# Kernel optimization log

Hardware: AMD Instinct MI355X
Metric: run time of the kernel (lower is better)

The kernel has to match this reference:

```python
import jax, jax.numpy as jnp
import numpy as np

PROJ_EPS = 4e-3      # geoopt-style Poincare projection margin (float32)
MIN_NORM = 1e-15
ATANH_EPS = 1e-5     # clamp arg of arctanh away from 1
WEI_EPS = 1e-3       # self.eps buffer
P_EXP = 2.0          # self.p buffer


def _project(v, k):
    # Project onto Poincare ball of curvature -k: clip norm to (1-eps)/sqrt(k).
    # k has shape (1,H,1,1), v has shape (B,H,T,D).
    maxnorm = (1.0 - PROJ_EPS) / jnp.sqrt(k)
    norm = jnp.sqrt(jnp.clip(jnp.sum(v * v, axis=-1, keepdims=True), MIN_NORM))
    return jnp.where(norm > maxnorm, v / norm * maxnorm, v)


def setup_inputs() -> dict:
    key = jax.random.key(0)
    k1, k2, k3, k4 = jax.random.split(key, 4)
    B, T, C, H = 4, 1024, 768, 12
    x = jax.random.normal(k1, (B, T, C), dtype=jnp.float32)
    Wqkv = jax.random.normal(k2, (3 * C, C), dtype=jnp.float32) * (1.0 / np.sqrt(C))
    Wproj = jax.random.normal(k3, (C, C), dtype=jnp.float32) * (1.0 / np.sqrt(C))
    # learnable per-head curvature, init ~ exp(randn)*curvature (must be > 0)
    kcurv = jax.random.uniform(k4, (1, H, 1, 1), dtype=jnp.float32, minval=0.5, maxval=1.5)
    return {"x": x, "Wqkv": Wqkv, "Wproj": Wproj, "kcurv": kcurv}


def reference(x, Wqkv, Wproj, kcurv):
    B, T, C = x.shape
    H = kcurv.shape[1]
    D = C // H

    qkv = x @ Wqkv.T                                  # (B,T,3C)
    q, kx, v = jnp.split(qkv, 3, axis=-1)

    def to_heads(t):
        return t.reshape(B, T, H, D).transpose(0, 2, 1, 3)  # (B,H,T,D)

    q, kx, v = to_heads(q), to_heads(kx), to_heads(v)

    qp = _project(q, kcurv)
    kp = _project(kx, kcurv)

    # Poincare distance d(x,y) = (2/sqrt(k)) * artanh(sqrt(k)*||(-x) mobius+ y||).
    # mobius_add(-x,y) = (-(1-2k<x,y>+k|y|^2) x + (1-k|x|^2) y) / (1-2k<x,y>+k^2|x|^2|y|^2)
    # => ||num||^2 = A^2|x|^2 + Bc^2|y|^2 - 2*A*Bc*<x,y>, avoiding (B,H,T,T,D) tensors.
    x2 = jnp.sum(qp * qp, axis=-1)                    # (B,H,T)
    y2 = jnp.sum(kp * kp, axis=-1)                    # (B,H,T)
    xy = jnp.einsum('bhid,bhjd->bhij', qp, kp)        # (B,H,T,T)

    kc = kcurv                                        # (1,H,1,1) broadcasts to (B,H,T,T)
    x2i = x2[..., :, None]                            # (B,H,T,1)
    y2j = y2[..., None, :]                            # (B,H,1,T)

    A = 1.0 - 2.0 * kc * xy + kc * y2j
    Bc = 1.0 - kc * x2i
    num2 = A * A * x2i + Bc * Bc * y2j - 2.0 * A * Bc * xy
    denom = 1.0 - 2.0 * kc * xy + (kc * kc) * x2i * y2j
    madd_norm = jnp.sqrt(jnp.clip(num2, MIN_NORM)) / jnp.clip(denom, MIN_NORM)

    sk = jnp.sqrt(kc)
    dist = (2.0 / sk) * jnp.arctanh(jnp.clip(sk * madd_norm, 0.0, 1.0 - ATANH_EPS))

    wei = 1.0 / (WEI_EPS + dist ** P_EXP)             # (B,H,T,T)
    causal = jnp.tril(jnp.ones((T, T), dtype=bool))
    wei = jnp.where(causal, wei, 0.0)
    wei = wei / jnp.sum(wei, axis=-1, keepdims=True)

    y = jnp.einsum('bhij,bhjd->bhid', wei, v)         # (B,H,T,D)
    y = y.transpose(0, 2, 1, 3).reshape(B, T, C)
    return y @ Wproj.T
```

## Files before the change

### kernel.cpp

```cpp
#include <hip/hip_runtime.h>
#include <hip/hip_bf16.h>
#include <math.h>

#define PROJ_EPSF 0.004f
#define MIN_NORMF 1e-15f
#define ATANH_EPSF 1e-5f
#define WEI_EPSF 1e-3f
#define LN2F 0.69314718055994531f

#define TT 1024
#define CC 768
#define HH 12
#define BBATCH 4

typedef unsigned long long ull;
typedef __attribute__((ext_vector_type(4))) float f32x4;
typedef __attribute__((ext_vector_type(8))) short bf16x8;

#define MFMA(a, b, c) __builtin_amdgcn_mfma_f32_16x16x32_bf16(a, b, c, 0, 0, 0)

static __device__ __forceinline__ uint cvtpk(float a, float b) {
    uint r;
    asm("v_cvt_pk_bf16_f32 %0, %1, %2" : "=v"(r) : "v"(a), "v"(b));
    return r;
}
static __device__ __forceinline__ ushort f2bf(float f) {
    uint u = __float_as_uint(f);
    u += 0x7fffu + ((u >> 16) & 1u);
    return (ushort)(u >> 16);
}
static __device__ __forceinline__ float bf2f(ushort h) {
    return __uint_as_float(((uint)h) << 16);
}
static __device__ __forceinline__ void split4(const float4& f, ull& hp, ull& lp) {
    uint h01 = cvtpk(f.x, f.y), h23 = cvtpk(f.z, f.w);
    float r0 = f.x - __uint_as_float(h01 << 16);
    float r1 = f.y - __uint_as_float(h01 & 0xffff0000u);
    float r2 = f.z - __uint_as_float(h23 << 16);
    float r3 = f.w - __uint_as_float(h23 & 0xffff0000u);
    uint l01 = cvtpk(r0, r1), l23 = cvtpk(r2, r3);
    hp = ((ull)h23 << 32) | h01;
    lp = ((ull)l23 << 32) | l01;
}
union pk16 { bf16x8 v; ull u[2]; };
static __device__ __forceinline__ void gl_lds16(const void* g, void* l) {
    __builtin_amdgcn_global_load_lds(
        (const __attribute__((address_space(1))) unsigned int*)g,
        (__attribute__((address_space(3))) unsigned int*)l, 16, 0, 0);
}

__global__ __launch_bounds__(256) void wprep(const float* __restrict__ W,
                                             ushort* __restrict__ Wh,
                                             ushort* __restrict__ Wl, int n4) {
    int i = blockIdx.x * 256 + threadIdx.x;
    if (i < n4) {
        float4 f = ((const float4*)W)[i];
        ull hp, lp;
        split4(f, hp, lp);
        ((ull*)Wh)[i] = hp;
        ((ull*)Wl)[i] = lp;
    }
}

__global__ __launch_bounds__(256) void gemm_qkv(
        const float* __restrict__ x, const ushort* __restrict__ Wh,
        const ushort* __restrict__ Wl, const float* __restrict__ kcurv,
        ushort* __restrict__ qh, ushort* __restrict__ ql,
        ushort* __restrict__ kh, ushort* __restrict__ kl,
        ushort* __restrict__ vT, float* __restrict__ x2g,
        float* __restrict__ y2g) {
    __shared__ ushort Ah[64 * 64], Al[64 * 64], Bh[64 * 64], Bl[64 * 64];
    const int tid = threadIdx.x, lane = tid & 63, wv = tid >> 6;
    const int wr = wv >> 1, wc = wv & 1, lr = lane & 15, lg = lane >> 4;
    const int m0 = blockIdx.x * 128, n0 = blockIdx.y * 128;
    const bool isV = (n0 >= 2 * CC);

    const int arow = tid >> 1, akh = tid & 1;
    const float* Ap = x + (size_t)(m0 + arow) * CC + akh * 16;
    const int ap_ = arow >> 1;
    const int ag0 = 4 * (arow & 1) + 2 * akh;
    const int aoff0 = ap_ * 128 + ((ag0 ^ (ap_ & 7)) << 4);
    const int aoff1 = ap_ * 128 + (((ag0 + 1) ^ (ap_ & 7)) << 4);
    const int c0 = 2 * wv, c1 = 2 * wv + 1;
    const int p0 = 8 * c0 + (lane >> 3), q0 = (lane & 7) ^ (p0 & 7);
    const int p1 = 8 * c1 + (lane >> 3), q1 = (lane & 7) ^ (p1 & 7);
    const size_t bs0 = (size_t)(n0 + 2 * p0 + (q0 >> 2)) * CC + (q0 & 3) * 8;
    const size_t bs1 = (size_t)(n0 + 2 * p1 + (q1 >> 2)) * CC + (q1 & 3) * 8;
    const int goff = (((4 * (lr & 1) + lg) ^ ((lr >> 1) & 7)) << 4);
    const int pa = wr * 32 + (lr >> 1);
    const int pb = wc * 32 + (lr >> 1);

    f32x4 acc[4][4] = {};
    float4 av[4];
#pragma unroll
    for (int q = 0; q < 4; ++q) av[q] = *(const float4*)(Ap + 4 * q);

    for (int kk = 0; kk < CC; kk += 32) {
        __syncthreads();
        pk16 h, l;
        split4(av[0], h.u[0], l.u[0]);
        split4(av[1], h.u[1], l.u[1]);
        *(bf16x8*)((char*)Ah + aoff0) = h.v;
        if (!isV) *(bf16x8*)((char*)Al + aoff0) = l.v;
        split4(av[2], h.u[0], l.u[0]);
        split4(av[3], h.u[1], l.u[1]);
        *(bf16x8*)((char*)Ah + aoff1) = h.v;
        if (!isV) *(bf16x8*)((char*)Al + aoff1) = l.v;
        gl_lds16(Wh + bs0 + kk, (char*)Bh + c0 * 1024);
        gl_lds16(Wh + bs1 + kk, (char*)Bh + c1 * 1024);
        if (!isV) {
            gl_lds16(Wl + bs0 + kk, (char*)Bl + c0 * 1024);
            gl_lds16(Wl + bs1 + kk, (char*)Bl + c1 * 1024);
        }
        asm volatile("s_waitcnt vmcnt(0)" ::: "memory");
        __syncthreads();
        if (kk + 32 < CC)
#pragma unroll
            for (int q = 0; q < 4; ++q)
                av[q] = *(const float4*)(Ap + kk + 32 + 4 * q);
        if (!isV) {
            bf16x8 a_h[4], a_l[4];
#pragma unroll
            for (int m = 0; m < 4; ++m) {
                const int off = (pa + m * 8) * 128 + goff;
                a_h[m] = *(const bf16x8*)((char*)Ah + off);
                a_l[m] = *(const bf16x8*)((char*)Al + off);
            }
#pragma unroll
            for (int n = 0; n < 4; ++n) {
                const int off = (pb + n * 8) * 128 + goff;
                bf16x8 b_h = *(const bf16x8*)((char*)Bh + off);
                bf16x8 b_l = *(const bf16x8*)((char*)Bl + off);
#pragma unroll
                for (int m = 0; m < 4; ++m) {
                    acc[m][n] = MFMA(a_h[m], b_h, acc[m][n]);
                    acc[m][n] = MFMA(a_h[m], b_l, acc[m][n]);
                    acc[m][n] = MFMA(a_l[m], b_h, acc[m][n]);
                }
            }
        } else {
            bf16x8 a_h[4], b_h[4];
#pragma unroll
            for (int m = 0; m < 4; ++m)
                a_h[m] = *(const bf16x8*)((char*)Ah + (pa + m * 8) * 128 + goff);
#pragma unroll
            for (int n = 0; n < 4; ++n)
                b_h[n] = *(const bf16x8*)((char*)Bh + (pb + n * 8) * 128 + goff);
#pragma unroll
            for (int n = 0; n < 4; ++n)
#pragma unroll
                for (int m = 0; m < 4; ++m)
                    acc[n][m] = MFMA(b_h[n], a_h[m], acc[n][m]);
        }
    }
    if (isV) {
        const int hd = (n0 - 2 * CC) / 64 + wc;
#pragma unroll
        for (int n = 0; n < 4; ++n)
#pragma unroll
            for (int m = 0; m < 4; ++m)
#pragma unroll
                for (int r = 0; r < 4; ++r) {
                    const int dl = n * 16 + lg * 4 + r;
                    const int tok = m0 + wr * 64 + m * 16 + lr;
                    vT[(size_t)(hd * 64 + dl) * 4096 + tok] = f2bf(acc[n][m][r]);
                }
    } else {
        const bool isQ = (n0 < CC);
        const int hd = (isQ ? n0 : n0 - CC) / 64 + wc;
        ushort* ph = isQ ? qh : kh;
        ushort* pl = isQ ? ql : kl;
        float* sg = isQ ? x2g : y2g;
        const float kcv = kcurv[hd];
        const float mxn = (1.0f - PROJ_EPSF) / sqrtf(kcv);
        const float mxn2 = mxn * mxn;
#pragma unroll
        for (int m = 0; m < 4; ++m)
#pragma unroll
            for (int r = 0; r < 4; ++r) {
                float s = 0.f;
#pragma unroll
                for (int n = 0; n < 4; ++n) s = fmaf(acc[m][n][r], acc[m][n][r], s);
                s += __shfl_xor(s, 1);
                s += __shfl_xor(s, 2);
                s += __shfl_xor(s, 4);
                s += __shfl_xor(s, 8);
                float scale = 1.0f, x2v = s;
                if (s > mxn2) {
                    scale = mxn * __builtin_amdgcn_rcpf(sqrtf(s));
                    x2v = s * scale * scale;
                }
                const int tok = m0 + wr * 64 + m * 16 + lg * 4 + r;
                const size_t rowb = (size_t)tok * CC + (isQ ? n0 : n0 - CC) + wc * 64;
#pragma unroll
                for (int n = 0; n < 4; ++n) {
                    const float v = acc[m][n][r] * scale;
                    const ushort hb = f2bf(v);
                    ph[rowb + n * 16 + lr] = hb;
                    pl[rowb + n * 16 + lr] = f2bf(v - bf2f(hb));
                }
                if (lr == 0)
                    sg[(size_t)((tok >> 10) * HH + hd) * TT + (tok & 1023)] = x2v;
            }
    }
}

__global__ __launch_bounds__(128) void hyp_attn(
        const ushort* __restrict__ qh, const ushort* __restrict__ ql,
        const ushort* __restrict__ kh, const ushort* __restrict__ kl,
        const ushort* __restrict__ vT, const float* __restrict__ x2g,
        const float* __restrict__ y2g, const float* __restrict__ kcurv,
        ushort* __restrict__ yh, ushort* __restrict__ yl) {
    const int ib = (int)blockIdx.x;
    const int xcd = ib & 7, t = ib >> 3;
    const int tcr = t / 12;
    const int which = t - tcr * 12;
    const int g32 = (15 - tcr) * 2 + (which & 1);
    const int bh = (which >> 1) * 8 + xcd;
    const int b = bh / HH, h = bh - b * HH;
    const int tid = threadIdx.x, lane = tid & 63, wv = tid >> 6;
    const int lr = lane & 15, lg = lane >> 4;
    const int rg = g32 * 2 + wv;
    const int rgq = g32 >> 1;

    __shared__ char ldsK[2][16384];
    __shared__ char ldsV[8192];
    __shared__ ushort wtb[2][16 * 72];
    ushort* wtw = wtb[wv];

    const float kc = kcurv[h];
    const float sk = sqrtf(kc);
    const float distc = LN2F / sk;
    const float d2c = distc * distc;
    const float twokc = 2.0f * kc;
    const float cA = 1.0f - ATANH_EPSF;

    const size_t qrb = (size_t)(b * TT + rg * 16 + lr) * CC + h * 64 + lg * 8;
    const bf16x8 qH0 = *(const bf16x8*)(qh + qrb), qH1 = *(const bf16x8*)(qh + qrb + 32);
    const bf16x8 qL0 = *(const bf16x8*)(ql + qrb), qL1 = *(const bf16x8*)(ql + qrb + 32);
    const float4 x2v = *(const float4*)&x2g[(size_t)bh * TT + rg * 16 + lg * 4];
    const float x2a[4] = { x2v.x, x2v.y, x2v.z, x2v.w };
    float kx2[4], Bc[4], Bc2[4];
#pragma unroll
    for (int r = 0; r < 4; ++r) {
        kx2[r] = kc * x2a[r];
        Bc[r] = 1.0f - kx2[r];
        Bc2[r] = Bc[r] * Bc[r];
    }

    const int srow8 = lane >> 3;
    const int sgrp = (lane & 7) ^ (srow8 & 7);
    const int so0 = ((lg ^ (lr & 7)) << 4);
    const int so1 = (((4 + lg) ^ (lr & 7)) << 4);
    const int lro = lr << 7;

#define STAGE_K(BUF, J0)                                                          \
    { _Pragma("unroll") for (int c4 = 0; c4 < 4; ++c4) {                          \
        const int c = wv * 4 + c4;                                                \
        const size_t gsrc = (size_t)(b * TT + (J0) + c * 8 + srow8) * CC + h * 64 + sgrp * 8; \
        gl_lds16(kh + gsrc, (char*)(BUF) + c * 1024);                             \
        gl_lds16(kl + gsrc, (char*)(BUF) + 8192 + c * 1024);                      \
    } }
#define STAGE_V(J0)                                                               \
    { _Pragma("unroll") for (int c4 = 0; c4 < 4; ++c4) {                          \
        const int c = wv * 4 + c4;                                                \
        gl_lds16(vT + (size_t)(h * 64 + c * 8 + srow8) * 4096 + b * TT + (J0) + sgrp * 8, \
                 ldsV + c * 1024);                                                \
    } }

#define TRANSF(NN, SA, Y2R)                                                        \
    {                                                                              \
        const float ky2 = kc * (Y2R);                                              \
        const float p1 = 1.0f + ky2;                                               \
        const int jg = j0 + NN * 16 + lr;                                          \
        _Pragma("unroll") for (int r = 0; r < 4; ++r) {                            \
            const float xy = SA[r];                                                \
            const float t2 = twokc * xy;                                           \
            const float Aa = p1 - t2;                                              \
            const float dn = fmaxf(fmaf(kx2[r], ky2, 1.0f) - t2, MIN_NORMF);       \
            const float ABxy = Aa * (Bc[r] * xy);                                  \
            const float c1 = fmaf(Bc2[r], (Y2R), -2.0f * ABxy);                    \
            const float num2 = fmaf(Aa * Aa, x2a[r], c1);                          \
            const float s = sqrtf(fmaxf(num2, MIN_NORMF));                         \
            const float sm = fminf(sk * s, cA * dn);                               \
            const float L = __builtin_amdgcn_logf((dn + sm) *                      \
                                __builtin_amdgcn_rcpf(dn - sm));                   \
            float w = __builtin_amdgcn_rcpf(fmaf(L * L, d2c, WEI_EPSF));           \
            if (mk && (jg > rg * 16 + lg * 4 + r)) w = 0.0f;                       \
            wtw[(lg * 4 + r) * 72 + NN * 16 + lr] = f2bf(w);                       \
            wsum[r] += w;                                                          \
        }                                                                          \
    }

    f32x4 pv[4] = {};
    float wsum[4] = {};

    STAGE_K(ldsK[0], 0)
    asm volatile("s_waitcnt vmcnt(0)" ::: "memory");
    __syncthreads();

    int cur = 0;
    for (int jt = 0; jt <= rgq; ++jt) {
        const int j0 = jt * 64;
        const bool mk = (jt == rgq);
        if (jt < rgq) STAGE_K(ldsK[cur ^ 1], j0 + 64)
        STAGE_V(j0)
        const size_t y2b = (size_t)bh * TT + j0 + lr;
        const float y2n[4] = { y2g[y2b], y2g[y2b + 16], y2g[y2b + 32], y2g[y2b + 48] };
        __builtin_amdgcn_s_setprio(1);
        f32x4 sacc[4] = {};
#pragma unroll
        for (int n = 0; n < 4; ++n) {
            const char* p = ldsK[cur] + n * 2048 + lro;
            bf16x8 h0 = *(const bf16x8*)(p + so0);
            bf16x8 h1 = *(const bf16x8*)(p + so1);
            bf16x8 l0 = *(const bf16x8*)(p + 8192 + so0);
            bf16x8 l1 = *(const bf16x8*)(p + 8192 + so1);
            sacc[n] = MFMA(qH0, h0, sacc[n]);
            sacc[n] = MFMA(qH0, l0, sacc[n]);
            sacc[n] = MFMA(qL0, h0, sacc[n]);
            sacc[n] = MFMA(qH1, h1, sacc[n]);
            sacc[n] = MFMA(qH1, l1, sacc[n]);
            sacc[n] = MFMA(qL1, h1, sacc[n]);
        }
        TRANSF(0, sacc[0], y2n[0])
        TRANSF(1, sacc[1], y2n[1])
        TRANSF(2, sacc[2], y2n[2])
        TRANSF(3, sacc[3], y2n[3])
        __builtin_amdgcn_s_setprio(0);
        asm volatile("s_waitcnt vmcnt(0)" ::: "memory");
        __syncthreads();
        __builtin_amdgcn_s_setprio(1);
        bf16x8 pw0 = *(const bf16x8*)&wtw[lr * 72 + lg * 8];
        bf16x8 pw1 = *(const bf16x8*)&wtw[lr * 72 + 32 + lg * 8];
#pragma unroll
        for (int n = 0; n < 4; ++n) {
            const char* p = ldsV + n * 2048 + lro;
            bf16x8 v0 = *(const bf16x8*)(p + so0);
            bf16x8 v1 = *(const bf16x8*)(p + so1);
            pv[n] = MFMA(pw0, v0, pv[n]);
            pv[n] = MFMA(pw1, v1, pv[n]);
        }
        __builtin_amdgcn_s_setprio(0);
        __syncthreads();
        cur ^= 1;
    }

    float den[4];
#pragma unroll
    for (int r = 0; r < 4; ++r) {
        float s = wsum[r];
        s += __shfl_xor(s, 1);
        s += __shfl_xor(s, 2);
        s += __shfl_xor(s, 4);
        s += __shfl_xor(s, 8);
        den[r] = s;
    }
#pragma unroll
    for (int r = 0; r < 4; ++r) {
        const float iv = __builtin_amdgcn_rcpf(den[r]);
        const size_t rowb = (size_t)(b * TT + rg * 16 + lg * 4 + r) * CC + h * 64;
#pragma unroll
        for (int n = 0; n < 4; ++n) {
            const float val = pv[n][r] * iv;
            const ushort hb = f2bf(val);
            yh[rowb + n * 16 + lr] = hb;
            yl[rowb + n * 16 + lr] = f2bf(val - bf2f(hb));
        }
    }
#undef TRANSF
#undef STAGE_K
#undef STAGE_V
}

__global__ __launch_bounds__(256) void gemm_out(const ushort* __restrict__ Ahp,
                                                const ushort* __restrict__ Alp,
                                                const ushort* __restrict__ Wh,
                                                const ushort* __restrict__ Wl,
                                                float* __restrict__ C) {
    __shared__ ushort Ah[32 * 64], Al[32 * 64], Bh[32 * 64], Bl[32 * 64];
    const int tid = threadIdx.x, lane = tid & 63, wv = tid >> 6;
    const int wr = wv >> 1, wc = wv & 1, lr = lane & 15, lg = lane >> 4;
    const int m0 = blockIdx.x * 64, n0 = blockIdx.y * 64;

    const int sp = 8 * wv + (lane >> 3);
    const int sg = (lane & 7) ^ (sp & 7);
    const int srow = 2 * sp + (sg >> 2);
    const int scol = (sg & 3) * 8;
    const size_t asrc = (size_t)(m0 + srow) * CC + scol;
    const size_t bsrc = (size_t)(n0 + srow) * CC + scol;
    const int goff = (((4 * (lr & 1) + lg) ^ ((lr >> 1) & 7)) << 4);
    const int pa = wr * 16 + (lr >> 1);
    const int pb = wc * 16 + (lr >> 1);

    f32x4 acc[2][2] = {};

    for (int kk = 0; kk < CC; kk += 32) {
        __syncthreads();
        gl_lds16(Ahp + asrc + kk, (char*)Ah + wv * 1024);
        gl_lds16(Alp + asrc + kk, (char*)Al + wv * 1024);
        gl_lds16(Wh + bsrc + kk, (char*)Bh + wv * 1024);
        gl_lds16(Wl + bsrc + kk, (char*)Bl + wv * 1024);
        asm volatile("s_waitcnt vmcnt(0)" ::: "memory");
        __syncthreads();
        bf16x8 a_h[2], a_l[2];
#pragma unroll
        for (int m = 0; m < 2; ++m) {
            const int off = (pa + m * 8) * 128 + goff;
            a_h[m] = *(const bf16x8*)((char*)Ah + off);
            a_l[m] = *(const bf16x8*)((char*)Al + off);
        }
#pragma unroll
        for (int n = 0; n < 2; ++n) {
            const int off = (pb + n * 8) * 128 + goff;
            bf16x8 b_h = *(const bf16x8*)((char*)Bh + off);
            bf16x8 b_l = *(const bf16x8*)((char*)Bl + off);
#pragma unroll
            for (int m = 0; m < 2; ++m) {
                acc[m][n] = MFMA(a_h[m], b_h, acc[m][n]);
                acc[m][n] = MFMA(a_h[m], b_l, acc[m][n]);
                acc[m][n] = MFMA(a_l[m], b_h, acc[m][n]);
            }
        }
    }
#pragma unroll
    for (int m = 0; m < 2; ++m)
#pragma unroll
        for (int n = 0; n < 2; ++n)
#pragma unroll
            for (int r = 0; r < 4; ++r)
                C[(size_t)(m0 + wr * 32 + m * 16 + lg * 4 + r) * CC + n0 + wc * 32 + n * 16 + lr] =
                    acc[m][n][r];
}

extern "C" void kernel_launch(void* const* d_in, const int* in_sizes, int n_in,
                              void* d_out, int out_size, void* d_ws, size_t ws_size,
                              hipStream_t stream) {
    const float* x     = (const float*)d_in[0];
    const float* Wqkv  = (const float*)d_in[1];
    const float* Wproj = (const float*)d_in[2];
    const float* kcurv = (const float*)d_in[3];
    float* out = (float*)d_out;

    const size_t PL = (size_t)4096 * CC;
    char* w = (char*)d_ws;
    ushort* Wqh = (ushort*)w;
    ushort* Wql = Wqh + (size_t)2304 * CC;
    ushort* yh  = (ushort*)w;
    ushort* yl  = yh + PL;
    ushort* qh  = (ushort*)(w + 2 * PL * 2);
    ushort* ql  = qh + PL;
    ushort* kh  = ql + PL;
    ushort* kl  = kh + PL;
    ushort* vT  = kl + PL;
    ushort* Wph = vT + PL;
    ushort* Wpl = Wph + (size_t)CC * CC;
    float* x2g  = (float*)(Wpl + (size_t)CC * CC);
    float* y2g  = x2g + 48 * TT;

    wprep<<<2304 * CC / 4 / 256, 256, 0, stream>>>(Wqkv, Wqh, Wql, 2304 * CC / 4);
    wprep<<<CC * CC / 4 / 256, 256, 0, stream>>>(Wproj, Wph, Wpl, CC * CC / 4);
    gemm_qkv<<<dim3(32, 18), 256, 0, stream>>>(x, Wqh, Wql, kcurv,
                                               qh, ql, kh, kl, vT, x2g, y2g);
    hyp_attn<<<1536, 128, 0, stream>>>(qh, ql, kh, kl, vT, x2g, y2g, kcurv, yh, yl);
    gemm_out<<<dim3(64, 12), 256, 0, stream>>>(yh, yl, Wph, Wpl, out);
}
```

Before: 156.1 us.

## Widen attention blocks to four waves and double-buffer output GEMM staging

The attention kernel now uses 256-thread blocks covering 64 query rows per block, so each staged K/V tile is shared by four waves instead of two, and half as many blocks are launched. Full vmcnt(0) waits plus __syncthreads are replaced by partial vmcnt counts and raw s_barrier, letting the next K tile load while the current one is computed. The output projection GEMM gains double-buffered LDS, prefetching the next k-slice while MFMAs run on the current one. The aim is to reduce redundant global loads and hide load latency, at the cost of more LDS and fewer blocks for load balancing. The hand-counted vmcnt values carry correctness risk if the instruction counts are off.

Result: faster. 143.3 us (-8.2%).

```diff
diff --git a/kernel.cpp b/kernel.cpp
--- a/kernel.cpp
+++ b/kernel.cpp
@@ -205,7 +205,7 @@
     }
 }
 
-__global__ __launch_bounds__(128) void hyp_attn(
+__global__ __launch_bounds__(256) void hyp_attn(
         const ushort* __restrict__ qh, const ushort* __restrict__ ql,
         const ushort* __restrict__ kh, const ushort* __restrict__ kl,
         const ushort* __restrict__ vT, const float* __restrict__ x2g,
@@ -213,19 +213,19 @@
         ushort* __restrict__ yh, ushort* __restrict__ yl) {
     const int ib = (int)blockIdx.x;
     const int xcd = ib & 7, t = ib >> 3;
-    const int tcr = t / 12;
-    const int which = t - tcr * 12;
-    const int g32 = (15 - tcr) * 2 + (which & 1);
-    const int bh = (which >> 1) * 8 + xcd;
+    const int tcr = t / 6;
+    const int which = t - tcr * 6;
+    const int g64 = 15 - tcr;
+    const int bh = which * 8 + xcd;
     const int b = bh / HH, h = bh - b * HH;
     const int tid = threadIdx.x, lane = tid & 63, wv = tid >> 6;
     const int lr = lane & 15, lg = lane >> 4;
-    const int rg = g32 * 2 + wv;
-    const int rgq = g32 >> 1;
+    const int rg = g64 * 4 + wv;
+    const int rgq = g64;
 
     __shared__ char ldsK[2][16384];
     __shared__ char ldsV[8192];
-    __shared__ ushort wtb[2][16 * 72];
+    __shared__ ushort wtb[4][16 * 72];
     ushort* wtw = wtb[wv];
 
     const float kc = kcurv[h];
@@ -255,15 +255,15 @@
     const int lro = lr << 7;
 
 #define STAGE_K(BUF, J0)                                                          \
-    { _Pragma("unroll") for (int c4 = 0; c4 < 4; ++c4) {                          \
-        const int c = wv * 4 + c4;                                                \
+    { _Pragma("unroll") for (int c4 = 0; c4 < 2; ++c4) {                          \
+        const int c = wv * 2 + c4;                                                \
         const size_t gsrc = (size_t)(b * TT + (J0) + c * 8 + srow8) * CC + h * 64 + sgrp * 8; \
         gl_lds16(kh + gsrc, (char*)(BUF) + c * 1024);                             \
         gl_lds16(kl + gsrc, (char*)(BUF) + 8192 + c * 1024);                      \
     } }
 #define STAGE_V(J0)                                                               \
-    { _Pragma("unroll") for (int c4 = 0; c4 < 4; ++c4) {                          \
-        const int c = wv * 4 + c4;                                                \
+    { _Pragma("unroll") for (int c4 = 0; c4 < 2; ++c4) {                          \
+        const int c = wv * 2 + c4;                                                \
         gl_lds16(vT + (size_t)(h * 64 + c * 8 + srow8) * 4096 + b * TT + (J0) + sgrp * 8, \
                  ldsV + c * 1024);                                                \
     } }
@@ -296,15 +296,20 @@
     float wsum[4] = {};
 
     STAGE_K(ldsK[0], 0)
-    asm volatile("s_waitcnt vmcnt(0)" ::: "memory");
-    __syncthreads();
 
     int cur = 0;
     for (int jt = 0; jt <= rgq; ++jt) {
         const int j0 = jt * 64;
         const bool mk = (jt == rgq);
-        if (jt < rgq) STAGE_K(ldsK[cur ^ 1], j0 + 64)
         STAGE_V(j0)
+        if (jt < rgq) {
+            STAGE_K(ldsK[cur ^ 1], j0 + 64)
+            asm volatile("s_waitcnt vmcnt(6)" ::: "memory");
+        } else {
+            asm volatile("s_waitcnt vmcnt(2)" ::: "memory");
+        }
+        __builtin_amdgcn_s_barrier();
+        __builtin_amdgcn_sched_barrier(0);
         const size_t y2b = (size_t)bh * TT + j0 + lr;
         const float y2n[4] = { y2g[y2b], y2g[y2b + 16], y2g[y2b + 32], y2g[y2b + 48] };
         __builtin_amdgcn_s_setprio(1);
@@ -328,8 +333,12 @@
         TRANSF(2, sacc[2], y2n[2])
         TRANSF(3, sacc[3], y2n[3])
         __builtin_amdgcn_s_setprio(0);
-        asm volatile("s_waitcnt vmcnt(0)" ::: "memory");
-        __syncthreads();
+        if (jt < rgq)
+            asm volatile("s_waitcnt vmcnt(4)" ::: "memory");
+        else
+            asm volatile("s_waitcnt vmcnt(0)" ::: "memory");
+        __builtin_amdgcn_s_barrier();
+        __builtin_amdgcn_sched_barrier(0);
         __builtin_amdgcn_s_setprio(1);
         bf16x8 pw0 = *(const bf16x8*)&wtw[lr * 72 + lg * 8];
         bf16x8 pw1 = *(const bf16x8*)&wtw[lr * 72 + 32 + lg * 8];
@@ -342,7 +351,7 @@
             pv[n] = MFMA(pw1, v1, pv[n]);
         }
         __builtin_amdgcn_s_setprio(0);
-        __syncthreads();
+        __builtin_amdgcn_s_barrier();
         cur ^= 1;
     }
 
@@ -378,7 +387,7 @@
                                                 const ushort* __restrict__ Wh,
                                                 const ushort* __restrict__ Wl,
                                                 float* __restrict__ C) {
-    __shared__ ushort Ah[32 * 64], Al[32 * 64], Bh[32 * 64], Bl[32 * 64];
+    __shared__ ushort Ah[2][32 * 64], Al[2][32 * 64], Bh[2][32 * 64], Bl[2][32 * 64];
     const int tid = threadIdx.x, lane = tid & 63, wv = tid >> 6;
     const int wr = wv >> 1, wc = wv & 1, lr = lane & 15, lg = lane >> 4;
     const int m0 = blockIdx.x * 64, n0 = blockIdx.y * 64;
@@ -395,26 +404,35 @@
 
     f32x4 acc[2][2] = {};
 
+#define STAGE_O(BUF, KK)                                                          \
+    gl_lds16(Ahp + asrc + (KK), (char*)Ah[BUF] + wv * 1024);                      \
+    gl_lds16(Alp + asrc + (KK), (char*)Al[BUF] + wv * 1024);                      \
+    gl_lds16(Wh + bsrc + (KK), (char*)Bh[BUF] + wv * 1024);                       \
+    gl_lds16(Wl + bsrc + (KK), (char*)Bl[BUF] + wv * 1024);
+
+    STAGE_O(0, 0)
+    int cur = 0;
     for (int kk = 0; kk < CC; kk += 32) {
-        __syncthreads();
-        gl_lds16(Ahp + asrc + kk, (char*)Ah + wv * 1024);
-        gl_lds16(Alp + asrc + kk, (char*)Al + wv * 1024);
-        gl_lds16(Wh + bsrc + kk, (char*)Bh + wv * 1024);
-        gl_lds16(Wl + bsrc + kk, (char*)Bl + wv * 1024);
-        asm volatile("s_waitcnt vmcnt(0)" ::: "memory");
-        __syncthreads();
+        if (kk + 32 < CC) {
+            STAGE_O(cur ^ 1, kk + 32)
+            asm volatile("s_waitcnt vmcnt(4)" ::: "memory");
+        } else {
+            asm volatile("s_waitcnt vmcnt(0)" ::: "memory");
+        }
+        __builtin_amdgcn_s_barrier();
+        __builtin_amdgcn_sched_barrier(0);
         bf16x8 a_h[2], a_l[2];
 #pragma unroll
         for (int m = 0; m < 2; ++m) {
             const int off = (pa + m * 8) * 128 + goff;
-            a_h[m] = *(const bf16x8*)((char*)Ah + off);
-            a_l[m] = *(const bf16x8*)((char*)Al + off);
+            a_h[m] = *(const bf16x8*)((char*)Ah[cur] + off);
+            a_l[m] = *(const bf16x8*)((char*)Al[cur] + off);
         }
 #pragma unroll
         for (int n = 0; n < 2; ++n) {
             const int off = (pb + n * 8) * 128 + goff;
-            bf16x8 b_h = *(const bf16x8*)((char*)Bh + off);
-            bf16x8 b_l = *(const bf16x8*)((char*)Bl + off);
+            bf16x8 b_h = *(const bf16x8*)((char*)Bh[cur] + off);
+            bf16x8 b_l = *(const bf16x8*)((char*)Bl[cur] + off);
 #pragma unroll
             for (int m = 0; m < 2; ++m) {
                 acc[m][n] = MFMA(a_h[m], b_h, acc[m][n]);
@@ -422,7 +440,10 @@
                 acc[m][n] = MFMA(a_l[m], b_h, acc[m][n]);
             }
         }
-    }
+        __builtin_amdgcn_s_barrier();
+        cur ^= 1;
+    }
+#undef STAGE_O
 #pragma unroll
     for (int m = 0; m < 2; ++m)
 #pragma unroll
@@ -462,6 +483,6 @@
     wprep<<<CC * CC / 4 / 256, 256, 0, stream>>>(Wproj, Wph, Wpl, CC * CC / 4);
     gemm_qkv<<<dim3(32, 18), 256, 0, stream>>>(x, Wqh, Wql, kcurv,
                                                qh, ql, kh, kl, vT, x2g, y2g);
-    hyp_attn<<<1536, 128, 0, stream>>>(qh, ql, kh, kl, vT, x2g, y2g, kcurv, yh, yl);
+    hyp_attn<<<768, 256, 0, stream>>>(qh, ql, kh, kl, vT, x2g, y2g, kcurv, yh, yl);
     gemm_out<<<dim3(64, 12), 256, 0, stream>>>(yh, yl, Wph, Wpl, out);
 }
```
